# Performance work log

Hardware: AMD Instinct MI355X
Metric: run time of the kernel (lower is better)

Reference implementation:

```python
import jax, jax.numpy as jnp
import numpy as np

N_HEAD = 16


def setup_inputs() -> dict:
    key = jax.random.key(0)
    ks = jax.random.split(key, 4)
    B, S, E = 1, 4096, 1024
    x = jax.random.normal(ks[0], (B, S, E), dtype=jnp.float32)
    # causal mask: True where attention is DISALLOWED (upper triangle)
    masked_matrix = ~jnp.tril(jnp.ones((S, S), dtype=bool))[None, None]
    Wqkv = jax.random.normal(ks[1], (E, 3 * E), dtype=jnp.float32) * (1.0 / np.sqrt(E))
    bqkv = jnp.zeros((3 * E,), dtype=jnp.float32)
    Wp = jax.random.normal(ks[2], (E, E), dtype=jnp.float32) * (1.0 / np.sqrt(E))
    bp = jnp.zeros((E,), dtype=jnp.float32)
    return {"x": x, "masked_matrix": masked_matrix, "Wqkv": Wqkv, "bqkv": bqkv,
            "Wp": Wp, "bp": bp}


def reference(x, masked_matrix, Wqkv, bqkv, Wp, bp):
    B, S, E = x.shape
    H = N_HEAD
    D = E // H
    qkv = x @ Wqkv + bqkv                        # [B,S,3E]
    q, k, v = jnp.split(qkv, 3, axis=-1)
    q = q.reshape(B, S, H, D).transpose(0, 2, 1, 3)  # [B,H,S,D]
    k = k.reshape(B, S, H, D).transpose(0, 2, 1, 3)
    v = v.reshape(B, S, H, D).transpose(0, 2, 1, 3)
    # NOTE: source applies NO 1/sqrt(D) scaling — kept faithful.
    att = jnp.einsum('bhqd,bhkd->bhqk', q, k)    # [B,H,S,S]
    att = jnp.where(masked_matrix, jnp.float32(-jnp.inf), att)
    att = jax.nn.softmax(att, axis=-1)
    res = jnp.einsum('bhqk,bhkd->bhqd', att, v)  # [B,H,S,D]
    res = res.transpose(0, 2, 1, 3).reshape(B, S, E)
    return res @ Wp + bp
```

## Files before the change

kernel.cpp:

```cpp
#include <hip/hip_runtime.h>
#include <hip/hip_bf16.h>
#include <math.h>

#define S_LEN 4096
#define EMB   1024
#define NHEAD 16
#define HDIM  64

typedef __attribute__((ext_vector_type(8))) _Float16 half8;
typedef __attribute__((ext_vector_type(4))) _Float16 half4;
typedef __attribute__((ext_vector_type(4))) float float4_t;
typedef __attribute__((ext_vector_type(16))) float float16_t;
typedef __attribute__((ext_vector_type(4))) int int4_t;
typedef __attribute__((ext_vector_type(2))) int int2_t;

#define GLOBAL_AS(p) ((const __attribute__((address_space(1))) void*)(p))
#define LDS_AS(p)    ((__attribute__((address_space(3))) void*)(p))

#define LOG2E 1.4426950408889634f

__global__ __launch_bounds__(256) void prep(
    const float* __restrict__ x, const float* __restrict__ Wqkv,
    const float* __restrict__ Wp,
    _Float16* __restrict__ xh, _Float16* __restrict__ WTh,
    _Float16* __restrict__ WpT)
{
    const int bid = blockIdx.x;
    if (bid < 4096) {
        const int i = bid * 256 + threadIdx.x;
        const float4_t v = ((const float4_t*)x)[i];
        half4 hh;
#pragma unroll
        for (int j = 0; j < 4; ++j) hh[j] = (_Float16)v[j];
        ((half4*)xh)[i] = hh;
        return;
    }
    __shared__ float t[64][65];
    const float* in;
    _Float16* out;
    int R, C, bx, by;
    if (bid < 4096 + 768) {
        const int idx = bid - 4096;
        bx = idx % 48; by = idx / 48;
        in = Wqkv; out = WTh; R = 1024; C = 3072;
    } else {
        const int idx = bid - 4864;
        bx = idx & 15; by = idx >> 4;
        in = Wp; out = WpT; R = 1024; C = 1024;
    }
    const int r0 = by * 64, c0 = bx * 64;
    for (int i = threadIdx.x; i < 64 * 64; i += 256) {
        int r = i >> 6, c = i & 63;
        t[r][c] = in[(size_t)(r0 + r) * C + c0 + c];
    }
    __syncthreads();
    for (int i = threadIdx.x; i < 64 * 64; i += 256) {
        int c = i >> 6, r = i & 63;
        out[(size_t)(c0 + c) * R + r0 + r] = (_Float16)t[r][c];
    }
}

__global__ __launch_bounds__(256) void gemm_qkv(
    const _Float16* __restrict__ Ag, const _Float16* __restrict__ Bg,
    const float* __restrict__ bias,
    _Float16* __restrict__ qk, _Float16* __restrict__ vt, int K)
{
    constexpr int BK = 32;
    __shared__ _Float16 Ah[128 * BK];
    __shared__ _Float16 Bh[128 * BK];

    const int tid = threadIdx.x;
    const int wave = tid >> 6, lane = tid & 63;
    const int l16 = lane & 15, quad = lane >> 4;
    const int wr = wave >> 1, wc = wave & 1;
    const int row0 = blockIdx.y * 128, col0 = blockIdx.x * 128;
    const int lrow = lane >> 2, lc8 = (lane & 3) * 8;

    float4_t acc[4][4];
#pragma unroll
    for (int i = 0; i < 4; ++i)
#pragma unroll
        for (int j = 0; j < 4; ++j) acc[i][j] = (float4_t){0.f, 0.f, 0.f, 0.f};

    for (int k0 = 0; k0 < K; k0 += BK) {
        __syncthreads();
#pragma unroll
        for (int i = 0; i < 2; ++i) {
            const int ar = i * 64 + wave * 16;
            __builtin_amdgcn_global_load_lds(
                GLOBAL_AS(Ag + (size_t)(row0 + ar + lrow) * K + k0 + lc8),
                LDS_AS(&Ah[ar * BK]), 16, 0, 0);
            __builtin_amdgcn_global_load_lds(
                GLOBAL_AS(Bg + (size_t)(col0 + ar + lrow) * K + k0 + lc8),
                LDS_AS(&Bh[ar * BK]), 16, 0, 0);
        }
        __syncthreads();

        half8 af[4], bfr[4];
#pragma unroll
        for (int t = 0; t < 4; ++t) {
            af[t]  = *(const half8*)&Ah[(wr * 64 + t * 16 + l16) * BK + quad * 8];
            bfr[t] = *(const half8*)&Bh[(wc * 64 + t * 16 + l16) * BK + quad * 8];
        }
#pragma unroll
        for (int i = 0; i < 4; ++i)
#pragma unroll
            for (int j = 0; j < 4; ++j)
                acc[i][j] = __builtin_amdgcn_mfma_f32_16x16x32_f16(af[i], bfr[j], acc[i][j], 0, 0, 0);
    }

#pragma unroll
    for (int i = 0; i < 4; ++i) {
#pragma unroll
        for (int j = 0; j < 4; ++j) {
            const int colb = col0 + wc * 64 + j * 16 + l16;
            const float bv = bias[colb];
            const int rowb = row0 + wr * 64 + i * 16 + quad * 4;
            if (colb < 2048) {
                const float sc = (colb >= 1024) ? LOG2E : 1.0f;
#pragma unroll
                for (int r = 0; r < 4; ++r)
                    qk[(size_t)(rowb + r) * 2048 + colb] =
                        (_Float16)((acc[i][j][r] + bv) * sc);
            } else {
                half4 w;
#pragma unroll
                for (int r = 0; r < 4; ++r) w[r] = (_Float16)(acc[i][j][r] + bv);
                *(half4*)&vt[(size_t)(colb - 2048) * 4096 + rowb] = w;
            }
        }
    }
}

__global__ __launch_bounds__(256) void gemm_out(
    const _Float16* __restrict__ Ag, const _Float16* __restrict__ Bg,
    const float* __restrict__ bias, float* __restrict__ C, int N, int K)
{
    constexpr int BK = 32;
    __shared__ _Float16 Ah[128 * BK];
    __shared__ _Float16 Bh[64 * BK];

    const int tid = threadIdx.x;
    const int wave = tid >> 6, lane = tid & 63;
    const int l16 = lane & 15, quad = lane >> 4;
    const int row0 = blockIdx.y * 128, col0 = blockIdx.x * 64;
    const int lrow = lane >> 2, lc8 = (lane & 3) * 8;

    float4_t acc[2][4];
#pragma unroll
    for (int i = 0; i < 2; ++i)
#pragma unroll
        for (int j = 0; j < 4; ++j) acc[i][j] = (float4_t){0.f, 0.f, 0.f, 0.f};

    for (int k0 = 0; k0 < K; k0 += BK) {
        __syncthreads();
#pragma unroll
        for (int i = 0; i < 2; ++i) {
            const int ar = i * 64 + wave * 16;
            __builtin_amdgcn_global_load_lds(
                GLOBAL_AS(Ag + (size_t)(row0 + ar + lrow) * K + k0 + lc8),
                LDS_AS(&Ah[ar * BK]), 16, 0, 0);
        }
        {
            const int br = wave * 16;
            __builtin_amdgcn_global_load_lds(
                GLOBAL_AS(Bg + (size_t)(col0 + br + lrow) * K + k0 + lc8),
                LDS_AS(&Bh[br * BK]), 16, 0, 0);
        }
        __syncthreads();

        half8 af[2], bfr[4];
#pragma unroll
        for (int t = 0; t < 2; ++t)
            af[t] = *(const half8*)&Ah[(wave * 32 + t * 16 + l16) * BK + quad * 8];
#pragma unroll
        for (int t = 0; t < 4; ++t)
            bfr[t] = *(const half8*)&Bh[(t * 16 + l16) * BK + quad * 8];
#pragma unroll
        for (int i = 0; i < 2; ++i)
#pragma unroll
            for (int j = 0; j < 4; ++j)
                acc[i][j] = __builtin_amdgcn_mfma_f32_16x16x32_f16(af[i], bfr[j], acc[i][j], 0, 0, 0);
    }

#pragma unroll
    for (int i = 0; i < 2; ++i) {
#pragma unroll
        for (int j = 0; j < 4; ++j) {
            const int colb = col0 + j * 16 + l16;
            const float bv = bias[colb];
#pragma unroll
            for (int r = 0; r < 4; ++r) {
                const int row = row0 + wave * 32 + i * 16 + quad * 4 + r;
                C[(size_t)row * N + colb] = acc[i][j][r] + bv;
            }
        }
    }
}

__global__ __launch_bounds__(256, 5) void flash_attn_f16(
    const _Float16* __restrict__ qk, const _Float16* __restrict__ v_t,
    _Float16* __restrict__ opart, float* __restrict__ mlpart)
{
    __shared__ __align__(16) _Float16 KsT[2][64 * 64];
    __shared__ __align__(16) _Float16 VtT[2][64 * 64];

    const int bid  = blockIdx.x;
    const int hv   = bid & 15;
    const int h    = (hv & 7) * 2 + (hv >> 3);
    const int idx  = bid >> 4;
    const int tile = 31 - (idx >> 2);
    const int split= idx & 3;
    const int dlen = 2 * tile + 1 - split;
    const int L    = (dlen < 0) ? 0 : (dlen >> 2) + 1;

    const int wave = threadIdx.x >> 6;
    const int lane = threadIdx.x & 63;
    const int l31  = lane & 31;
    const int hi   = lane >> 5;

    const int dma_r = wave * 16 + (lane >> 3);
    const int dma_c = ((lane & 7) ^ (lane >> 3)) * 8;

    const _Float16* kplane = qk + 1024 + h * HDIM;
    const _Float16* vplane = v_t + (size_t)h * HDIM * 4096;

    const int q0 = tile * 128 + wave * 32;

    half8 qf[4];
#pragma unroll
    for (int jj = 0; jj < 4; ++jj)
        qf[jj] = *(const half8*)(qk + (size_t)(q0 + l31) * 2048 + h * HDIM
                                 + jj * 16 + hi * 8);

    float16_t o0 = (float16_t)0.f, o1 = (float16_t)0.f;
    float m_r = -INFINITY, l_r = 0.f;

    if (L > 0) {
        const int kb0 = 64 * split;
#pragma unroll
        for (int p = 0; p < 2; ++p) {
            const int r = dma_r + p * 8;
            __builtin_amdgcn_global_load_lds(
                GLOBAL_AS(kplane + (size_t)(kb0 + r) * 2048 + dma_c),
                LDS_AS(&KsT[0][(wave * 128 + p * 64) * 8]), 16, 0, 0);
            __builtin_amdgcn_global_load_lds(
                GLOBAL_AS(vplane + (size_t)r * 4096 + kb0 + dma_c),
                LDS_AS(&VtT[0][(wave * 128 + p * 64) * 8]), 16, 0, 0);
        }

        int ib = 0;
        int kb = kb0;
        for (int it = 0; it < L; ++it, kb += 256, ib ^= 1) {
            __syncthreads();

            if (it < L - 1) {
                const int kn = kb + 256;
#pragma unroll
                for (int p = 0; p < 2; ++p) {
                    const int r = dma_r + p * 8;
                    __builtin_amdgcn_global_load_lds(
                        GLOBAL_AS(kplane + (size_t)(kn + r) * 2048 + dma_c),
                        LDS_AS(&KsT[ib ^ 1][(wave * 128 + p * 64) * 8]), 16, 0, 0);
                    __builtin_amdgcn_global_load_lds(
                        GLOBAL_AS(vplane + (size_t)r * 4096 + kn + dma_c),
                        LDS_AS(&VtT[ib ^ 1][(wave * 128 + p * 64) * 8]), 16, 0, 0);
                }
            }

            if (kb <= q0 + 31) {
                float16_t s0 = (float16_t)0.f, s1 = (float16_t)0.f;
                __builtin_amdgcn_s_setprio(1);
#pragma unroll
                for (int jj = 0; jj < 4; ++jj) {
                    const int r7 = l31 & 7;
                    const half8 kf0 = *(const half8*)&KsT[ib][
                        ((l31) * 8 + ((2 * jj + hi) ^ r7)) * 8];
                    const half8 kf1 = *(const half8*)&KsT[ib][
                        ((32 + l31) * 8 + ((2 * jj + hi) ^ r7)) * 8];
                    s0 = __builtin_amdgcn_mfma_f32_32x32x16_f16(kf0, qf[jj], s0, 0, 0, 0);
                    s1 = __builtin_amdgcn_mfma_f32_32x32x16_f16(kf1, qf[jj], s1, 0, 0, 0);
                }
                __builtin_amdgcn_s_setprio(0);

                if (kb + 63 > q0) {
                    const int qg = q0 + l31;
#pragma unroll
                    for (int gg = 0; gg < 4; ++gg)
#pragma unroll
                        for (int r = 0; r < 4; ++r) {
                            const int keyb = kb + r + 8 * gg + 4 * hi;
                            if (keyb > qg)      s0[4 * gg + r] = -INFINITY;
                            if (keyb + 32 > qg) s1[4 * gg + r] = -INFINITY;
                        }
                }

                float mx = s0[0];
#pragma unroll
                for (int i = 1; i < 16; ++i) mx = fmaxf(mx, s0[i]);
#pragma unroll
                for (int i = 0; i < 16; ++i) mx = fmaxf(mx, s1[i]);
                mx = fmaxf(mx, __shfl_xor(mx, 32));
                const bool  grow  = mx > m_r + 8.0f;
                const float mnew  = grow ? mx : m_r;
                const float alpha = __builtin_amdgcn_exp2f(m_r - mnew);

                int w0[8], w1[8];
                float lsum = 0.f;
#pragma unroll
                for (int i = 0; i < 8; ++i) {
                    const float pa = __builtin_amdgcn_exp2f(s0[2 * i]     - mnew);
                    const float pb = __builtin_amdgcn_exp2f(s0[2 * i + 1] - mnew);
                    lsum += pa + pb;
                    w0[i] = __builtin_bit_cast(int, __builtin_amdgcn_cvt_pkrtz(pa, pb));
                }
#pragma unroll
                for (int i = 0; i < 8; ++i) {
                    const float pa = __builtin_amdgcn_exp2f(s1[2 * i]     - mnew);
                    const float pb = __builtin_amdgcn_exp2f(s1[2 * i + 1] - mnew);
                    lsum += pa + pb;
                    w1[i] = __builtin_bit_cast(int, __builtin_amdgcn_cvt_pkrtz(pa, pb));
                }
                l_r = l_r * alpha + lsum;
                m_r = mnew;
                if (__any(grow)) {
#pragma unroll
                    for (int i = 0; i < 16; ++i) { o0[i] *= alpha; o1[i] *= alpha; }
                }

                half8 pf[4];
                {
                    const int2_t a02 = __builtin_amdgcn_permlane32_swap(w0[0], w0[2], 0, 0);
                    const int2_t a13 = __builtin_amdgcn_permlane32_swap(w0[1], w0[3], 0, 0);
                    const int2_t a46 = __builtin_amdgcn_permlane32_swap(w0[4], w0[6], 0, 0);
                    const int2_t a57 = __builtin_amdgcn_permlane32_swap(w0[5], w0[7], 0, 0);
                    int4_t f0 = {a02[0], a13[0], a02[1], a13[1]};
                    int4_t f1 = {a46[0], a57[0], a46[1], a57[1]};
                    pf[0] = __builtin_bit_cast(half8, f0);
                    pf[1] = __builtin_bit_cast(half8, f1);
                    const int2_t b02 = __builtin_amdgcn_permlane32_swap(w1[0], w1[2], 0, 0);
                    const int2_t b13 = __builtin_amdgcn_permlane32_swap(w1[1], w1[3], 0, 0);
                    const int2_t b46 = __builtin_amdgcn_permlane32_swap(w1[4], w1[6], 0, 0);
                    const int2_t b57 = __builtin_amdgcn_permlane32_swap(w1[5], w1[7], 0, 0);
                    int4_t f2 = {b02[0], b13[0], b02[1], b13[1]};
                    int4_t f3 = {b46[0], b57[0], b46[1], b57[1]};
                    pf[2] = __builtin_bit_cast(half8, f2);
                    pf[3] = __builtin_bit_cast(half8, f3);
                }

                __builtin_amdgcn_s_setprio(1);
#pragma unroll
                for (int kc = 0; kc < 4; ++kc) {
                    const int r7 = l31 & 7;
                    const half8 vf0 = *(const half8*)&VtT[ib][
                        ((l31) * 8 + ((2 * kc + hi) ^ r7)) * 8];
                    const half8 vf1 = *(const half8*)&VtT[ib][
                        ((32 + l31) * 8 + ((2 * kc + hi) ^ r7)) * 8];
                    o0 = __builtin_amdgcn_mfma_f32_32x32x16_f16(vf0, pf[kc], o0, 0, 0, 0);
                    o1 = __builtin_amdgcn_mfma_f32_32x32x16_f16(vf1, pf[kc], o1, 0, 0, 0);
                }
                __builtin_amdgcn_s_setprio(0);
            }
        }
    }

    const float lr = l_r + __shfl_xor(l_r, 32);
    const size_t prow = (size_t)(split * 4096 + q0 + l31);
#pragma unroll
    for (int gg = 0; gg < 4; ++gg) {
        half4 wa, wb;
#pragma unroll
        for (int r = 0; r < 4; ++r) {
            wa[r] = (_Float16)o0[4 * gg + r];
            wb[r] = (_Float16)o1[4 * gg + r];
        }
        const size_t base = prow * 1024 + h * HDIM + 8 * gg + 4 * hi;
        *(half4*)&opart[base]      = wa;
        *(half4*)&opart[base + 32] = wb;
    }
    if (hi == 0) {
        float2 ml; ml.x = m_r; ml.y = lr;
        ((float2*)mlpart)[prow * 16 + h] = ml;
    }
}

__global__ __launch_bounds__(256) void combine(
    const _Float16* __restrict__ opart, const float* __restrict__ mlpart,
    _Float16* __restrict__ resh)
{
    const int idx = blockIdx.x * 256 + threadIdx.x;
    const int row = idx >> 7;
    const int c8  = (idx & 127) * 8;
    const int h   = c8 >> 6;
    float2 ml[4];
#pragma unroll
    for (int s = 0; s < 4; ++s)
        ml[s] = ((const float2*)mlpart)[(size_t)(s * 4096 + row) * 16 + h];
    const float m = fmaxf(fmaxf(ml[0].x, ml[1].x), fmaxf(ml[2].x, ml[3].x));
    float a[4], lsum = 0.f;
#pragma unroll
    for (int s = 0; s < 4; ++s) {
        a[s] = __builtin_amdgcn_exp2f(ml[s].x - m);
        lsum += ml[s].y * a[s];
    }
    const float inv = 1.0f / lsum;
    float acc[8];
#pragma unroll
    for (int jj = 0; jj < 8; ++jj) acc[jj] = 0.f;
#pragma unroll
    for (int s = 0; s < 4; ++s) {
        const half8 os = *(const half8*)&opart[(size_t)(s * 4096 + row) * 1024 + c8];
#pragma unroll
        for (int jj = 0; jj < 8; ++jj) acc[jj] += (float)os[jj] * a[s];
    }
    half8 w;
#pragma unroll
    for (int jj = 0; jj < 8; ++jj) w[jj] = (_Float16)(acc[jj] * inv);
    *(half8*)&resh[(size_t)row * 1024 + c8] = w;
}

extern "C" void kernel_launch(void* const* d_in, const int* in_sizes, int n_in,
                              void* d_out, int out_size, void* d_ws, size_t ws_size,
                              hipStream_t stream)
{
    const float* x    = (const float*)d_in[0];
    const float* Wqkv = (const float*)d_in[2];
    const float* bqkv = (const float*)d_in[3];
    const float* Wp   = (const float*)d_in[4];
    const float* bp   = (const float*)d_in[5];
    float* out = (float*)d_out;

    _Float16* xh  = (_Float16*)d_ws;
    _Float16* WTh = xh + (size_t)4096 * 1024;
    _Float16* qkh = WTh + (size_t)3072 * 1024;
    _Float16* vtg = qkh + (size_t)4096 * 2048;
    _Float16* WpT = vtg + (size_t)1024 * 4096;
    _Float16* opart = WpT + (size_t)1024 * 1024;
    float* mlpart = (float*)(opart + (size_t)4 * 4096 * 1024);
    _Float16* resh = xh;

    dim3 blk(256);

    prep<<<dim3(5120), blk, 0, stream>>>(x, Wqkv, Wp, xh, WTh, WpT);

    gemm_qkv<<<dim3(3072 / 128, 4096 / 128), blk, 0, stream>>>(
        xh, WTh, bqkv, qkh, vtg, 1024);

    flash_attn_f16<<<dim3(2048), dim3(256), 0, stream>>>(qkh, vtg, opart, mlpart);

    combine<<<dim3(2048), blk, 0, stream>>>(opart, mlpart, resh);

    gemm_out<<<dim3(1024 / 64, 4096 / 128), blk, 0, stream>>>(
        resh, WpT, bp, out, 1024, 1024);
}
```

Before: 272.9 us.

## Split attention KV by contiguous chunks via lookup table, skip unused partials

Replaces the interleaved 4-way split of keys (stride 256) with contiguous key chunks of up to 1024 keys, scheduled through a constant table that encodes tile, chunk index and length, ordered longest-first. The grid shrinks from 2048 to 1280 blocks, and the combine kernel only reads as many partials as a row actually has. Each block now walks adjacent 64-key blocks, which should improve locality and drop the idle blocks of the old split, at the cost of a hand-built table and less even per-block work.

After: 298.3 us. 1.09x slower.

```diff
diff --git a/kernel.cpp b/kernel.cpp
--- a/kernel.cpp
+++ b/kernel.cpp
@@ -198,6 +198,34 @@
     }
 }
 
+__device__ __constant__ unsigned short CHUNKS[80] = {
+    2079, 2111, 2143, 2175,
+    2078, 2110, 2142,
+    2077, 2109, 2141,
+    2076, 2108, 2140,
+    2075, 2107, 2139,
+    2074, 2106, 2138,
+    2073, 2105, 2137,
+    2072, 2104, 2136,
+    2071, 2103, 2135,
+    2070, 2102,
+    2069, 2101,
+    2068, 2100,
+    2067, 2099,
+    2066, 2098,
+    2065, 2097,
+    2064, 2096,
+    2063, 2095,
+    2062, 2061, 2060, 2059, 2058, 2057, 2056, 2055,
+    1918, 1878, 1838, 1798,
+    1661, 1621, 1581, 1541,
+    1404, 1364, 1324, 1284,
+    1147, 1107, 1067, 1027,
+     890,  850,  810,  770,
+     633,  593,  553,  513,
+     376,  336,  296,  256
+};
+
 __global__ __launch_bounds__(256, 5) void flash_attn_f16(
     const _Float16* __restrict__ qk, const _Float16* __restrict__ v_t,
     _Float16* __restrict__ opart, float* __restrict__ mlpart)
@@ -208,11 +236,10 @@
     const int bid  = blockIdx.x;
     const int hv   = bid & 15;
     const int h    = (hv & 7) * 2 + (hv >> 3);
-    const int idx  = bid >> 4;
-    const int tile = 31 - (idx >> 2);
-    const int split= idx & 3;
-    const int dlen = 2 * tile + 1 - split;
-    const int L    = (dlen < 0) ? 0 : (dlen >> 2) + 1;
+    const int e    = CHUNKS[bid >> 4];
+    const int tile = e & 31;
+    const int jch  = (e >> 5) & 3;
+    const int L    = e >> 7;
 
     const int wave = threadIdx.x >> 6;
     const int lane = threadIdx.x & 63;
@@ -236,136 +263,134 @@
     float16_t o0 = (float16_t)0.f, o1 = (float16_t)0.f;
     float m_r = -INFINITY, l_r = 0.f;
 
-    if (L > 0) {
-        const int kb0 = 64 * split;
-#pragma unroll
-        for (int p = 0; p < 2; ++p) {
-            const int r = dma_r + p * 8;
-            __builtin_amdgcn_global_load_lds(
-                GLOBAL_AS(kplane + (size_t)(kb0 + r) * 2048 + dma_c),
-                LDS_AS(&KsT[0][(wave * 128 + p * 64) * 8]), 16, 0, 0);
-            __builtin_amdgcn_global_load_lds(
-                GLOBAL_AS(vplane + (size_t)r * 4096 + kb0 + dma_c),
-                LDS_AS(&VtT[0][(wave * 128 + p * 64) * 8]), 16, 0, 0);
-        }
-
-        int ib = 0;
-        int kb = kb0;
-        for (int it = 0; it < L; ++it, kb += 256, ib ^= 1) {
-            __syncthreads();
-
-            if (it < L - 1) {
-                const int kn = kb + 256;
-#pragma unroll
-                for (int p = 0; p < 2; ++p) {
-                    const int r = dma_r + p * 8;
-                    __builtin_amdgcn_global_load_lds(
-                        GLOBAL_AS(kplane + (size_t)(kn + r) * 2048 + dma_c),
-                        LDS_AS(&KsT[ib ^ 1][(wave * 128 + p * 64) * 8]), 16, 0, 0);
-                    __builtin_amdgcn_global_load_lds(
-                        GLOBAL_AS(vplane + (size_t)r * 4096 + kn + dma_c),
-                        LDS_AS(&VtT[ib ^ 1][(wave * 128 + p * 64) * 8]), 16, 0, 0);
-                }
-            }
-
-            if (kb <= q0 + 31) {
-                float16_t s0 = (float16_t)0.f, s1 = (float16_t)0.f;
-                __builtin_amdgcn_s_setprio(1);
-#pragma unroll
-                for (int jj = 0; jj < 4; ++jj) {
-                    const int r7 = l31 & 7;
-                    const half8 kf0 = *(const half8*)&KsT[ib][
-                        ((l31) * 8 + ((2 * jj + hi) ^ r7)) * 8];
-                    const half8 kf1 = *(const half8*)&KsT[ib][
-                        ((32 + l31) * 8 + ((2 * jj + hi) ^ r7)) * 8];
-                    s0 = __builtin_amdgcn_mfma_f32_32x32x16_f16(kf0, qf[jj], s0, 0, 0, 0);
-                    s1 = __builtin_amdgcn_mfma_f32_32x32x16_f16(kf1, qf[jj], s1, 0, 0, 0);
-                }
-                __builtin_amdgcn_s_setprio(0);
-
-                if (kb + 63 > q0) {
-                    const int qg = q0 + l31;
-#pragma unroll
-                    for (int gg = 0; gg < 4; ++gg)
-#pragma unroll
-                        for (int r = 0; r < 4; ++r) {
-                            const int keyb = kb + r + 8 * gg + 4 * hi;
-                            if (keyb > qg)      s0[4 * gg + r] = -INFINITY;
-                            if (keyb + 32 > qg) s1[4 * gg + r] = -INFINITY;
-                        }
-                }
-
-                float mx = s0[0];
-#pragma unroll
-                for (int i = 1; i < 16; ++i) mx = fmaxf(mx, s0[i]);
-#pragma unroll
-                for (int i = 0; i < 16; ++i) mx = fmaxf(mx, s1[i]);
-                mx = fmaxf(mx, __shfl_xor(mx, 32));
-                const bool  grow  = mx > m_r + 8.0f;
-                const float mnew  = grow ? mx : m_r;
-                const float alpha = __builtin_amdgcn_exp2f(m_r - mnew);
-
-                int w0[8], w1[8];
-                float lsum = 0.f;
-#pragma unroll
-                for (int i = 0; i < 8; ++i) {
-                    const float pa = __builtin_amdgcn_exp2f(s0[2 * i]     - mnew);
-                    const float pb = __builtin_amdgcn_exp2f(s0[2 * i + 1] - mnew);
-                    lsum += pa + pb;
-                    w0[i] = __builtin_bit_cast(int, __builtin_amdgcn_cvt_pkrtz(pa, pb));
-                }
-#pragma unroll
-                for (int i = 0; i < 8; ++i) {
-                    const float pa = __builtin_amdgcn_exp2f(s1[2 * i]     - mnew);
-                    const float pb = __builtin_amdgcn_exp2f(s1[2 * i + 1] - mnew);
-                    lsum += pa + pb;
-                    w1[i] = __builtin_bit_cast(int, __builtin_amdgcn_cvt_pkrtz(pa, pb));
-                }
-                l_r = l_r * alpha + lsum;
-                m_r = mnew;
-                if (__any(grow)) {
-#pragma unroll
-                    for (int i = 0; i < 16; ++i) { o0[i] *= alpha; o1[i] *= alpha; }
-                }
-
-                half8 pf[4];
-                {
-                    const int2_t a02 = __builtin_amdgcn_permlane32_swap(w0[0], w0[2], 0, 0);
-                    const int2_t a13 = __builtin_amdgcn_permlane32_swap(w0[1], w0[3], 0, 0);
-                    const int2_t a46 = __builtin_amdgcn_permlane32_swap(w0[4], w0[6], 0, 0);
-                    const int2_t a57 = __builtin_amdgcn_permlane32_swap(w0[5], w0[7], 0, 0);
-                    int4_t f0 = {a02[0], a13[0], a02[1], a13[1]};
-                    int4_t f1 = {a46[0], a57[0], a46[1], a57[1]};
-                    pf[0] = __builtin_bit_cast(half8, f0);
-                    pf[1] = __builtin_bit_cast(half8, f1);
-                    const int2_t b02 = __builtin_amdgcn_permlane32_swap(w1[0], w1[2], 0, 0);
-                    const int2_t b13 = __builtin_amdgcn_permlane32_swap(w1[1], w1[3], 0, 0);
-                    const int2_t b46 = __builtin_amdgcn_permlane32_swap(w1[4], w1[6], 0, 0);
-                    const int2_t b57 = __builtin_amdgcn_permlane32_swap(w1[5], w1[7], 0, 0);
-                    int4_t f2 = {b02[0], b13[0], b02[1], b13[1]};
-                    int4_t f3 = {b46[0], b57[0], b46[1], b57[1]};
-                    pf[2] = __builtin_bit_cast(half8, f2);
-                    pf[3] = __builtin_bit_cast(half8, f3);
-                }
-
-                __builtin_amdgcn_s_setprio(1);
-#pragma unroll
-                for (int kc = 0; kc < 4; ++kc) {
-                    const int r7 = l31 & 7;
-                    const half8 vf0 = *(const half8*)&VtT[ib][
-                        ((l31) * 8 + ((2 * kc + hi) ^ r7)) * 8];
-                    const half8 vf1 = *(const half8*)&VtT[ib][
-                        ((32 + l31) * 8 + ((2 * kc + hi) ^ r7)) * 8];
-                    o0 = __builtin_amdgcn_mfma_f32_32x32x16_f16(vf0, pf[kc], o0, 0, 0, 0);
-                    o1 = __builtin_amdgcn_mfma_f32_32x32x16_f16(vf1, pf[kc], o1, 0, 0, 0);
-                }
-                __builtin_amdgcn_s_setprio(0);
-            }
+    const int kb0 = jch << 10;
+#pragma unroll
+    for (int p = 0; p < 2; ++p) {
+        const int r = dma_r + p * 8;
+        __builtin_amdgcn_global_load_lds(
+            GLOBAL_AS(kplane + (size_t)(kb0 + r) * 2048 + dma_c),
+            LDS_AS(&KsT[0][(wave * 128 + p * 64) * 8]), 16, 0, 0);
+        __builtin_amdgcn_global_load_lds(
+            GLOBAL_AS(vplane + (size_t)r * 4096 + kb0 + dma_c),
+            LDS_AS(&VtT[0][(wave * 128 + p * 64) * 8]), 16, 0, 0);
+    }
+
+    int ib = 0;
+    int kb = kb0;
+    for (int it = 0; it < L; ++it, kb += 64, ib ^= 1) {
+        __syncthreads();
+
+        if (it < L - 1) {
+            const int kn = kb + 64;
+#pragma unroll
+            for (int p = 0; p < 2; ++p) {
+                const int r = dma_r + p * 8;
+                __builtin_amdgcn_global_load_lds(
+                    GLOBAL_AS(kplane + (size_t)(kn + r) * 2048 + dma_c),
+                    LDS_AS(&KsT[ib ^ 1][(wave * 128 + p * 64) * 8]), 16, 0, 0);
+                __builtin_amdgcn_global_load_lds(
+                    GLOBAL_AS(vplane + (size_t)r * 4096 + kn + dma_c),
+                    LDS_AS(&VtT[ib ^ 1][(wave * 128 + p * 64) * 8]), 16, 0, 0);
+            }
+        }
+
+        if (kb <= q0 + 31) {
+            float16_t s0 = (float16_t)0.f, s1 = (float16_t)0.f;
+            __builtin_amdgcn_s_setprio(1);
+#pragma unroll
+            for (int jj = 0; jj < 4; ++jj) {
+                const int r7 = l31 & 7;
+                const half8 kf0 = *(const half8*)&KsT[ib][
+                    ((l31) * 8 + ((2 * jj + hi) ^ r7)) * 8];
+                const half8 kf1 = *(const half8*)&KsT[ib][
+                    ((32 + l31) * 8 + ((2 * jj + hi) ^ r7)) * 8];
+                s0 = __builtin_amdgcn_mfma_f32_32x32x16_f16(kf0, qf[jj], s0, 0, 0, 0);
+                s1 = __builtin_amdgcn_mfma_f32_32x32x16_f16(kf1, qf[jj], s1, 0, 0, 0);
+            }
+            __builtin_amdgcn_s_setprio(0);
+
+            if (kb + 63 > q0) {
+                const int qg = q0 + l31;
+#pragma unroll
+                for (int gg = 0; gg < 4; ++gg)
+#pragma unroll
+                    for (int r = 0; r < 4; ++r) {
+                        const int keyb = kb + r + 8 * gg + 4 * hi;
+                        if (keyb > qg)      s0[4 * gg + r] = -INFINITY;
+                        if (keyb + 32 > qg) s1[4 * gg + r] = -INFINITY;
+                    }
+            }
+
+            float mx = s0[0];
+#pragma unroll
+            for (int i = 1; i < 16; ++i) mx = fmaxf(mx, s0[i]);
+#pragma unroll
+            for (int i = 0; i < 16; ++i) mx = fmaxf(mx, s1[i]);
+            mx = fmaxf(mx, __shfl_xor(mx, 32));
+            const bool  grow  = mx > m_r + 8.0f;
+            const float mnew  = grow ? mx : m_r;
+            const float alpha = __builtin_amdgcn_exp2f(m_r - mnew);
+
+            int w0[8], w1[8];
+            float lsum = 0.f;
+#pragma unroll
+            for (int i = 0; i < 8; ++i) {
+                const float pa = __builtin_amdgcn_exp2f(s0[2 * i]     - mnew);
+                const float pb = __builtin_amdgcn_exp2f(s0[2 * i + 1] - mnew);
+                lsum += pa + pb;
+                w0[i] = __builtin_bit_cast(int, __builtin_amdgcn_cvt_pkrtz(pa, pb));
+            }
+#pragma unroll
+            for (int i = 0; i < 8; ++i) {
+                const float pa = __builtin_amdgcn_exp2f(s1[2 * i]     - mnew);
+                const float pb = __builtin_amdgcn_exp2f(s1[2 * i + 1] - mnew);
+                lsum += pa + pb;
+                w1[i] = __builtin_bit_cast(int, __builtin_amdgcn_cvt_pkrtz(pa, pb));
+            }
+            l_r = l_r * alpha + lsum;
+            m_r = mnew;
+            if (__any(grow)) {
+#pragma unroll
+                for (int i = 0; i < 16; ++i) { o0[i] *= alpha; o1[i] *= alpha; }
+            }
+
+            half8 pf[4];
+            {
+                const int2_t a02 = __builtin_amdgcn_permlane32_swap(w0[0], w0[2], 0, 0);
+                const int2_t a13 = __builtin_amdgcn_permlane32_swap(w0[1], w0[3], 0, 0);
+                const int2_t a46 = __builtin_amdgcn_permlane32_swap(w0[4], w0[6], 0, 0);
+                const int2_t a57 = __builtin_amdgcn_permlane32_swap(w0[5], w0[7], 0, 0);
+                int4_t f0 = {a02[0], a13[0], a02[1], a13[1]};
+                int4_t f1 = {a46[0], a57[0], a46[1], a57[1]};
+                pf[0] = __builtin_bit_cast(half8, f0);
+                pf[1] = __builtin_bit_cast(half8, f1);
+                const int2_t b02 = __builtin_amdgcn_permlane32_swap(w1[0], w1[2], 0, 0);
+                const int2_t b13 = __builtin_amdgcn_permlane32_swap(w1[1], w1[3], 0, 0);
+                const int2_t b46 = __builtin_amdgcn_permlane32_swap(w1[4], w1[6], 0, 0);
+                const int2_t b57 = __builtin_amdgcn_permlane32_swap(w1[5], w1[7], 0, 0);
+                int4_t f2 = {b02[0], b13[0], b02[1], b13[1]};
+                int4_t f3 = {b46[0], b57[0], b46[1], b57[1]};
+                pf[2] = __builtin_bit_cast(half8, f2);
+                pf[3] = __builtin_bit_cast(half8, f3);
+            }
+
+            __builtin_amdgcn_s_setprio(1);
+#pragma unroll
+            for (int kc = 0; kc < 4; ++kc) {
+                const int r7 = l31 & 7;
+                const half8 vf0 = *(const half8*)&VtT[ib][
+                    ((l31) * 8 + ((2 * kc + hi) ^ r7)) * 8];
+                const half8 vf1 = *(const half8*)&VtT[ib][
+                    ((32 + l31) * 8 + ((2 * kc + hi) ^ r7)) * 8];
+                o0 = __builtin_amdgcn_mfma_f32_32x32x16_f16(vf0, pf[kc], o0, 0, 0, 0);
+                o1 = __builtin_amdgcn_mfma_f32_32x32x16_f16(vf1, pf[kc], o1, 0, 0, 0);
+            }
+            __builtin_amdgcn_s_setprio(0);
         }
     }
 
     const float lr = l_r + __shfl_xor(l_r, 32);
-    const size_t prow = (size_t)(split * 4096 + q0 + l31);
+    const size_t prow = (size_t)(jch * 4096 + q0 + l31);
 #pragma unroll
     for (int gg = 0; gg < 4; ++gg) {
         half4 wa, wb;
@@ -392,14 +417,15 @@
     const int row = idx >> 7;
     const int c8  = (idx & 127) * 8;
     const int h   = c8 >> 6;
+    const int nch = ((row >> 7) + 8) >> 3;
     float2 ml[4];
-#pragma unroll
-    for (int s = 0; s < 4; ++s)
+    float m = -INFINITY;
+    for (int s = 0; s < nch; ++s) {
         ml[s] = ((const float2*)mlpart)[(size_t)(s * 4096 + row) * 16 + h];
-    const float m = fmaxf(fmaxf(ml[0].x, ml[1].x), fmaxf(ml[2].x, ml[3].x));
+        m = fmaxf(m, ml[s].x);
+    }
     float a[4], lsum = 0.f;
-#pragma unroll
-    for (int s = 0; s < 4; ++s) {
+    for (int s = 0; s < nch; ++s) {
         a[s] = __builtin_amdgcn_exp2f(ml[s].x - m);
         lsum += ml[s].y * a[s];
     }
@@ -407,8 +433,7 @@
     float acc[8];
 #pragma unroll
     for (int jj = 0; jj < 8; ++jj) acc[jj] = 0.f;
-#pragma unroll
-    for (int s = 0; s < 4; ++s) {
+    for (int s = 0; s < nch; ++s) {
         const half8 os = *(const half8*)&opart[(size_t)(s * 4096 + row) * 1024 + c8];
 #pragma unroll
         for (int jj = 0; jj < 8; ++jj) acc[jj] += (float)os[jj] * a[s];
@@ -446,7 +471,7 @@
     gemm_qkv<<<dim3(3072 / 128, 4096 / 128), blk, 0, stream>>>(
         xh, WTh, bqkv, qkh, vtg, 1024);
 
-    flash_attn_f16<<<dim3(2048), dim3(256), 0, stream>>>(qkh, vtg, opart, mlpart);
+    flash_attn_f16<<<dim3(1280), dim3(256), 0, stream>>>(qkh, vtg, opart, mlpart);
 
     combine<<<dim3(2048), blk, 0, stream>>>(opart, mlpart, resh);
 
```

## Pair causal tiles per block with contiguous key splits, swizzle GEMM block order

Applied to the files above, without the earlier changes.

The attention kernel now gives each block two query tiles (tile p and 31-p), so every block does the same amount of causal work. Each of the four splits covers a contiguous range of key chunks instead of a strided one, and the grid is halved to 1024 blocks with a lower occupancy hint. Both GEMMs remap block indices with a swizzle so that consecutively scheduled blocks fall in different row/column tiles, which is meant to spread work across XCDs and improve cache reuse. The risks are fewer resident blocks and a longer serial loop per block, and a split can now have zero chunks, so combine must handle a -inf max.

Result: faster. 251.4 us (-7.9%).

```diff
diff --git a/kernel.cpp b/kernel.cpp
--- a/kernel.cpp
+++ b/kernel.cpp
@@ -73,7 +73,9 @@
     const int wave = tid >> 6, lane = tid & 63;
     const int l16 = lane & 15, quad = lane >> 4;
     const int wr = wave >> 1, wc = wave & 1;
-    const int row0 = blockIdx.y * 128, col0 = blockIdx.x * 128;
+    const int lid = blockIdx.y * 24 + blockIdx.x;
+    const int swz = (lid & 7) * 96 + (lid >> 3);
+    const int row0 = (swz / 24) * 128, col0 = (swz % 24) * 128;
     const int lrow = lane >> 2, lc8 = (lane & 3) * 8;
 
     float4_t acc[4][4];
@@ -143,7 +145,9 @@
     const int tid = threadIdx.x;
     const int wave = tid >> 6, lane = tid & 63;
     const int l16 = lane & 15, quad = lane >> 4;
-    const int row0 = blockIdx.y * 128, col0 = blockIdx.x * 64;
+    const int lid = blockIdx.y * 16 + blockIdx.x;
+    const int swz = (lid & 7) * 64 + (lid >> 3);
+    const int row0 = (swz / 16) * 128, col0 = (swz % 16) * 64;
     const int lrow = lane >> 2, lc8 = (lane & 3) * 8;
 
     float4_t acc[2][4];
@@ -198,7 +202,7 @@
     }
 }
 
-__global__ __launch_bounds__(256, 5) void flash_attn_f16(
+__global__ __launch_bounds__(256, 4) void flash_attn_f16(
     const _Float16* __restrict__ qk, const _Float16* __restrict__ v_t,
     _Float16* __restrict__ opart, float* __restrict__ mlpart)
 {
@@ -208,11 +212,8 @@
     const int bid  = blockIdx.x;
     const int hv   = bid & 15;
     const int h    = (hv & 7) * 2 + (hv >> 3);
-    const int idx  = bid >> 4;
-    const int tile = 31 - (idx >> 2);
-    const int split= idx & 3;
-    const int dlen = 2 * tile + 1 - split;
-    const int L    = (dlen < 0) ? 0 : (dlen >> 2) + 1;
+    const int pp   = (bid >> 4) & 15;
+    const int sch  = bid >> 8;
 
     const int wave = threadIdx.x >> 6;
     const int lane = threadIdx.x & 63;
@@ -225,162 +226,169 @@
     const _Float16* kplane = qk + 1024 + h * HDIM;
     const _Float16* vplane = v_t + (size_t)h * HDIM * 4096;
 
-    const int q0 = tile * 128 + wave * 32;
-
-    half8 qf[4];
-#pragma unroll
-    for (int jj = 0; jj < 4; ++jj)
-        qf[jj] = *(const half8*)(qk + (size_t)(q0 + l31) * 2048 + h * HDIM
-                                 + jj * 16 + hi * 8);
-
-    float16_t o0 = (float16_t)0.f, o1 = (float16_t)0.f;
-    float m_r = -INFINITY, l_r = 0.f;
-
-    if (L > 0) {
-        const int kb0 = 64 * split;
-#pragma unroll
-        for (int p = 0; p < 2; ++p) {
-            const int r = dma_r + p * 8;
-            __builtin_amdgcn_global_load_lds(
-                GLOBAL_AS(kplane + (size_t)(kb0 + r) * 2048 + dma_c),
-                LDS_AS(&KsT[0][(wave * 128 + p * 64) * 8]), 16, 0, 0);
-            __builtin_amdgcn_global_load_lds(
-                GLOBAL_AS(vplane + (size_t)r * 4096 + kb0 + dma_c),
-                LDS_AS(&VtT[0][(wave * 128 + p * 64) * 8]), 16, 0, 0);
-        }
-
-        int ib = 0;
-        int kb = kb0;
-        for (int it = 0; it < L; ++it, kb += 256, ib ^= 1) {
+    for (int ph = 0; ph < 2; ++ph) {
+        const int tile = ph ? (31 - pp) : pp;
+        const int Nt   = 2 * tile + 2;
+        const int c0   = (sch * Nt) >> 2;
+        const int L    = (((sch + 1) * Nt) >> 2) - c0;
+        const int q0   = tile * 128 + wave * 32;
+
+        half8 qf[4];
+#pragma unroll
+        for (int jj = 0; jj < 4; ++jj)
+            qf[jj] = *(const half8*)(qk + (size_t)(q0 + l31) * 2048 + h * HDIM
+                                     + jj * 16 + hi * 8);
+
+        float16_t o0 = (float16_t)0.f, o1 = (float16_t)0.f;
+        float m_r = -INFINITY, l_r = 0.f;
+
+        if (L > 0) {
+            const int kb0 = c0 * 64;
             __syncthreads();
-
-            if (it < L - 1) {
-                const int kn = kb + 256;
-#pragma unroll
-                for (int p = 0; p < 2; ++p) {
-                    const int r = dma_r + p * 8;
-                    __builtin_amdgcn_global_load_lds(
-                        GLOBAL_AS(kplane + (size_t)(kn + r) * 2048 + dma_c),
-                        LDS_AS(&KsT[ib ^ 1][(wave * 128 + p * 64) * 8]), 16, 0, 0);
-                    __builtin_amdgcn_global_load_lds(
-                        GLOBAL_AS(vplane + (size_t)r * 4096 + kn + dma_c),
-                        LDS_AS(&VtT[ib ^ 1][(wave * 128 + p * 64) * 8]), 16, 0, 0);
+#pragma unroll
+            for (int p = 0; p < 2; ++p) {
+                const int r = dma_r + p * 8;
+                __builtin_amdgcn_global_load_lds(
+                    GLOBAL_AS(kplane + (size_t)(kb0 + r) * 2048 + dma_c),
+                    LDS_AS(&KsT[0][(wave * 128 + p * 64) * 8]), 16, 0, 0);
+                __builtin_amdgcn_global_load_lds(
+                    GLOBAL_AS(vplane + (size_t)r * 4096 + kb0 + dma_c),
+                    LDS_AS(&VtT[0][(wave * 128 + p * 64) * 8]), 16, 0, 0);
+            }
+
+            int ib = 0;
+            int kb = kb0;
+            for (int it = 0; it < L; ++it, kb += 64, ib ^= 1) {
+                __syncthreads();
+
+                if (it < L - 1) {
+                    const int kn = kb + 64;
+#pragma unroll
+                    for (int p = 0; p < 2; ++p) {
+                        const int r = dma_r + p * 8;
+                        __builtin_amdgcn_global_load_lds(
+                            GLOBAL_AS(kplane + (size_t)(kn + r) * 2048 + dma_c),
+                            LDS_AS(&KsT[ib ^ 1][(wave * 128 + p * 64) * 8]), 16, 0, 0);
+                        __builtin_amdgcn_global_load_lds(
+                            GLOBAL_AS(vplane + (size_t)r * 4096 + kn + dma_c),
+                            LDS_AS(&VtT[ib ^ 1][(wave * 128 + p * 64) * 8]), 16, 0, 0);
+                    }
+                }
+
+                if (kb <= q0 + 31) {
+                    float16_t s0 = (float16_t)0.f, s1 = (float16_t)0.f;
+                    __builtin_amdgcn_s_setprio(1);
+#pragma unroll
+                    for (int jj = 0; jj < 4; ++jj) {
+                        const int r7 = l31 & 7;
+                        const half8 kf0 = *(const half8*)&KsT[ib][
+                            ((l31) * 8 + ((2 * jj + hi) ^ r7)) * 8];
+                        const half8 kf1 = *(const half8*)&KsT[ib][
+                            ((32 + l31) * 8 + ((2 * jj + hi) ^ r7)) * 8];
+                        s0 = __builtin_amdgcn_mfma_f32_32x32x16_f16(kf0, qf[jj], s0, 0, 0, 0);
+                        s1 = __builtin_amdgcn_mfma_f32_32x32x16_f16(kf1, qf[jj], s1, 0, 0, 0);
+                    }
+                    __builtin_amdgcn_s_setprio(0);
+
+                    if (kb + 63 > q0) {
+                        const int qg = q0 + l31;
+#pragma unroll
+                        for (int gg = 0; gg < 4; ++gg)
+#pragma unroll
+                            for (int r = 0; r < 4; ++r) {
+                                const int keyb = kb + r + 8 * gg + 4 * hi;
+                                if (keyb > qg)      s0[4 * gg + r] = -INFINITY;
+                                if (keyb + 32 > qg) s1[4 * gg + r] = -INFINITY;
+                            }
+                    }
+
+                    float mx = s0[0];
+#pragma unroll
+                    for (int i = 1; i < 16; ++i) mx = fmaxf(mx, s0[i]);
+#pragma unroll
+                    for (int i = 0; i < 16; ++i) mx = fmaxf(mx, s1[i]);
+                    mx = fmaxf(mx, __shfl_xor(mx, 32));
+                    const bool  grow  = mx > m_r + 8.0f;
+                    const float mnew  = grow ? mx : m_r;
+                    const float alpha = __builtin_amdgcn_exp2f(m_r - mnew);
+
+                    int w0[8], w1[8];
+                    float lsum = 0.f;
+#pragma unroll
+                    for (int i = 0; i < 8; ++i) {
+                        const float pa = __builtin_amdgcn_exp2f(s0[2 * i]     - mnew);
+                        const float pb = __builtin_amdgcn_exp2f(s0[2 * i + 1] - mnew);
+                        lsum += pa + pb;
+                        w0[i] = __builtin_bit_cast(int, __builtin_amdgcn_cvt_pkrtz(pa, pb));
+                    }
+#pragma unroll
+                    for (int i = 0; i < 8; ++i) {
+                        const float pa = __builtin_amdgcn_exp2f(s1[2 * i]     - mnew);
+                        const float pb = __builtin_amdgcn_exp2f(s1[2 * i + 1] - mnew);
+                        lsum += pa + pb;
+                        w1[i] = __builtin_bit_cast(int, __builtin_amdgcn_cvt_pkrtz(pa, pb));
+                    }
+                    l_r = l_r * alpha + lsum;
+                    m_r = mnew;
+                    if (__any(grow)) {
+#pragma unroll
+                        for (int i = 0; i < 16; ++i) { o0[i] *= alpha; o1[i] *= alpha; }
+                    }
+
+                    half8 pf[4];
+                    {
+                        const int2_t a02 = __builtin_amdgcn_permlane32_swap(w0[0], w0[2], 0, 0);
+                        const int2_t a13 = __builtin_amdgcn_permlane32_swap(w0[1], w0[3], 0, 0);
+                        const int2_t a46 = __builtin_amdgcn_permlane32_swap(w0[4], w0[6], 0, 0);
+                        const int2_t a57 = __builtin_amdgcn_permlane32_swap(w0[5], w0[7], 0, 0);
+                        int4_t f0 = {a02[0], a13[0], a02[1], a13[1]};
+                        int4_t f1 = {a46[0], a57[0], a46[1], a57[1]};
+                        pf[0] = __builtin_bit_cast(half8, f0);
+                        pf[1] = __builtin_bit_cast(half8, f1);
+                        const int2_t b02 = __builtin_amdgcn_permlane32_swap(w1[0], w1[2], 0, 0);
+                        const int2_t b13 = __builtin_amdgcn_permlane32_swap(w1[1], w1[3], 0, 0);
+                        const int2_t b46 = __builtin_amdgcn_permlane32_swap(w1[4], w1[6], 0, 0);
+                        const int2_t b57 = __builtin_amdgcn_permlane32_swap(w1[5], w1[7], 0, 0);
+                        int4_t f2 = {b02[0], b13[0], b02[1], b13[1]};
+                        int4_t f3 = {b46[0], b57[0], b46[1], b57[1]};
+                        pf[2] = __builtin_bit_cast(half8, f2);
+                        pf[3] = __builtin_bit_cast(half8, f3);
+                    }
+
+                    __builtin_amdgcn_s_setprio(1);
+#pragma unroll
+                    for (int kc = 0; kc < 4; ++kc) {
+                        const int r7 = l31 & 7;
+                        const half8 vf0 = *(const half8*)&VtT[ib][
+                            ((l31) * 8 + ((2 * kc + hi) ^ r7)) * 8];
+                        const half8 vf1 = *(const half8*)&VtT[ib][
+                            ((32 + l31) * 8 + ((2 * kc + hi) ^ r7)) * 8];
+                        o0 = __builtin_amdgcn_mfma_f32_32x32x16_f16(vf0, pf[kc], o0, 0, 0, 0);
+                        o1 = __builtin_amdgcn_mfma_f32_32x32x16_f16(vf1, pf[kc], o1, 0, 0, 0);
+                    }
+                    __builtin_amdgcn_s_setprio(0);
                 }
             }
-
-            if (kb <= q0 + 31) {
-                float16_t s0 = (float16_t)0.f, s1 = (float16_t)0.f;
-                __builtin_amdgcn_s_setprio(1);
-#pragma unroll
-                for (int jj = 0; jj < 4; ++jj) {
-                    const int r7 = l31 & 7;
-                    const half8 kf0 = *(const half8*)&KsT[ib][
-                        ((l31) * 8 + ((2 * jj + hi) ^ r7)) * 8];
-                    const half8 kf1 = *(const half8*)&KsT[ib][
-                        ((32 + l31) * 8 + ((2 * jj + hi) ^ r7)) * 8];
-                    s0 = __builtin_amdgcn_mfma_f32_32x32x16_f16(kf0, qf[jj], s0, 0, 0, 0);
-                    s1 = __builtin_amdgcn_mfma_f32_32x32x16_f16(kf1, qf[jj], s1, 0, 0, 0);
-                }
-                __builtin_amdgcn_s_setprio(0);
-
-                if (kb + 63 > q0) {
-                    const int qg = q0 + l31;
-#pragma unroll
-                    for (int gg = 0; gg < 4; ++gg)
-#pragma unroll
-                        for (int r = 0; r < 4; ++r) {
-                            const int keyb = kb + r + 8 * gg + 4 * hi;
-                            if (keyb > qg)      s0[4 * gg + r] = -INFINITY;
-                            if (keyb + 32 > qg) s1[4 * gg + r] = -INFINITY;
-                        }
-                }
-
-                float mx = s0[0];
-#pragma unroll
-                for (int i = 1; i < 16; ++i) mx = fmaxf(mx, s0[i]);
-#pragma unroll
-                for (int i = 0; i < 16; ++i) mx = fmaxf(mx, s1[i]);
-                mx = fmaxf(mx, __shfl_xor(mx, 32));
-                const bool  grow  = mx > m_r + 8.0f;
-                const float mnew  = grow ? mx : m_r;
-                const float alpha = __builtin_amdgcn_exp2f(m_r - mnew);
-
-                int w0[8], w1[8];
-                float lsum = 0.f;
-#pragma unroll
-                for (int i = 0; i < 8; ++i) {
-                    const float pa = __builtin_amdgcn_exp2f(s0[2 * i]     - mnew);
-                    const float pb = __builtin_amdgcn_exp2f(s0[2 * i + 1] - mnew);
-                    lsum += pa + pb;
-                    w0[i] = __builtin_bit_cast(int, __builtin_amdgcn_cvt_pkrtz(pa, pb));
-                }
-#pragma unroll
-                for (int i = 0; i < 8; ++i) {
-                    const float pa = __builtin_amdgcn_exp2f(s1[2 * i]     - mnew);
-                    const float pb = __builtin_amdgcn_exp2f(s1[2 * i + 1] - mnew);
-                    lsum += pa + pb;
-                    w1[i] = __builtin_bit_cast(int, __builtin_amdgcn_cvt_pkrtz(pa, pb));
-                }
-                l_r = l_r * alpha + lsum;
-                m_r = mnew;
-                if (__any(grow)) {
-#pragma unroll
-                    for (int i = 0; i < 16; ++i) { o0[i] *= alpha; o1[i] *= alpha; }
-                }
-
-                half8 pf[4];
-                {
-                    const int2_t a02 = __builtin_amdgcn_permlane32_swap(w0[0], w0[2], 0, 0);
-                    const int2_t a13 = __builtin_amdgcn_permlane32_swap(w0[1], w0[3], 0, 0);
-                    const int2_t a46 = __builtin_amdgcn_permlane32_swap(w0[4], w0[6], 0, 0);
-                    const int2_t a57 = __builtin_amdgcn_permlane32_swap(w0[5], w0[7], 0, 0);
-                    int4_t f0 = {a02[0], a13[0], a02[1], a13[1]};
-                    int4_t f1 = {a46[0], a57[0], a46[1], a57[1]};
-                    pf[0] = __builtin_bit_cast(half8, f0);
-                    pf[1] = __builtin_bit_cast(half8, f1);
-                    const int2_t b02 = __builtin_amdgcn_permlane32_swap(w1[0], w1[2], 0, 0);
-                    const int2_t b13 = __builtin_amdgcn_permlane32_swap(w1[1], w1[3], 0, 0);
-                    const int2_t b46 = __builtin_amdgcn_permlane32_swap(w1[4], w1[6], 0, 0);
-                    const int2_t b57 = __builtin_amdgcn_permlane32_swap(w1[5], w1[7], 0, 0);
-                    int4_t f2 = {b02[0], b13[0], b02[1], b13[1]};
-                    int4_t f3 = {b46[0], b57[0], b46[1], b57[1]};
-                    pf[2] = __builtin_bit_cast(half8, f2);
-                    pf[3] = __builtin_bit_cast(half8, f3);
-                }
-
-                __builtin_amdgcn_s_setprio(1);
-#pragma unroll
-                for (int kc = 0; kc < 4; ++kc) {
-                    const int r7 = l31 & 7;
-                    const half8 vf0 = *(const half8*)&VtT[ib][
-                        ((l31) * 8 + ((2 * kc + hi) ^ r7)) * 8];
-                    const half8 vf1 = *(const half8*)&VtT[ib][
-                        ((32 + l31) * 8 + ((2 * kc + hi) ^ r7)) * 8];
-                    o0 = __builtin_amdgcn_mfma_f32_32x32x16_f16(vf0, pf[kc], o0, 0, 0, 0);
-                    o1 = __builtin_amdgcn_mfma_f32_32x32x16_f16(vf1, pf[kc], o1, 0, 0, 0);
-                }
-                __builtin_amdgcn_s_setprio(0);
+        }
+
+        const float lr = l_r + __shfl_xor(l_r, 32);
+        const size_t prow = (size_t)(sch * 4096 + q0 + l31);
+#pragma unroll
+        for (int gg = 0; gg < 4; ++gg) {
+            half4 wa, wb;
+#pragma unroll
+            for (int r = 0; r < 4; ++r) {
+                wa[r] = (_Float16)o0[4 * gg + r];
+                wb[r] = (_Float16)o1[4 * gg + r];
             }
-        }
-    }
-
-    const float lr = l_r + __shfl_xor(l_r, 32);
-    const size_t prow = (size_t)(split * 4096 + q0 + l31);
-#pragma unroll
-    for (int gg = 0; gg < 4; ++gg) {
-        half4 wa, wb;
-#pragma unroll
-        for (int r = 0; r < 4; ++r) {
-            wa[r] = (_Float16)o0[4 * gg + r];
-            wb[r] = (_Float16)o1[4 * gg + r];
-        }
-        const size_t base = prow * 1024 + h * HDIM + 8 * gg + 4 * hi;
-        *(half4*)&opart[base]      = wa;
-        *(half4*)&opart[base + 32] = wb;
-    }
-    if (hi == 0) {
-        float2 ml; ml.x = m_r; ml.y = lr;
-        ((float2*)mlpart)[prow * 16 + h] = ml;
+            const size_t base = prow * 1024 + h * HDIM + 8 * gg + 4 * hi;
+            *(half4*)&opart[base]      = wa;
+            *(half4*)&opart[base + 32] = wb;
+        }
+        if (hi == 0) {
+            float2 ml; ml.x = m_r; ml.y = lr;
+            ((float2*)mlpart)[prow * 16 + h] = ml;
+        }
     }
 }
 
@@ -393,10 +401,12 @@
     const int c8  = (idx & 127) * 8;
     const int h   = c8 >> 6;
     float2 ml[4];
-#pragma unroll
-    for (int s = 0; s < 4; ++s)
+    float m = -INFINITY;
+#pragma unroll
+    for (int s = 0; s < 4; ++s) {
         ml[s] = ((const float2*)mlpart)[(size_t)(s * 4096 + row) * 16 + h];
-    const float m = fmaxf(fmaxf(ml[0].x, ml[1].x), fmaxf(ml[2].x, ml[3].x));
+        m = fmaxf(m, ml[s].x);
+    }
     float a[4], lsum = 0.f;
 #pragma unroll
     for (int s = 0; s < 4; ++s) {
@@ -446,7 +456,7 @@
     gemm_qkv<<<dim3(3072 / 128, 4096 / 128), blk, 0, stream>>>(
         xh, WTh, bqkv, qkh, vtg, 1024);
 
-    flash_attn_f16<<<dim3(2048), dim3(256), 0, stream>>>(qkh, vtg, opart, mlpart);
+    flash_attn_f16<<<dim3(1024), dim3(256), 0, stream>>>(qkh, vtg, opart, mlpart);
 
     combine<<<dim3(2048), blk, 0, stream>>>(opart, mlpart, resh);
 
```
